# Kernel optimization log

Measured on AMD Instinct MI355X. Metric: run time of the kernel, lower is better.

The kernel has to match this reference:

```python
import jax, jax.numpy as jnp
import numpy as np

OUT = 3      # pooled output size (fmap_size//4 = 14//4 = 3)
RATIO = 2    # roi_align sampling ratio (fixed; torchvision adaptive ratio for 14/3 bins is 2)
P = 20       # num_persons


def _bilinear(fm, y, x):
    # fm: [C,H,W]; y,x broadcastable coordinate grids. torchvision aligned=False semantics.
    C, H, W = fm.shape
    y, x = jnp.broadcast_arrays(y, x)
    valid = (y > -1.0) & (y < H) & (x > -1.0) & (x < W)
    y = jnp.clip(y, 0.0, H - 1.0)
    x = jnp.clip(x, 0.0, W - 1.0)
    y0 = jnp.floor(y).astype(jnp.int32)
    x0 = jnp.floor(x).astype(jnp.int32)
    y1 = jnp.minimum(y0 + 1, H - 1)
    x1 = jnp.minimum(x0 + 1, W - 1)
    ly = y - y0
    lx = x - x0
    hy = 1.0 - ly
    hx = 1.0 - lx
    v00 = fm[:, y0, x0]
    v01 = fm[:, y0, x1]
    v10 = fm[:, y1, x0]
    v11 = fm[:, y1, x1]
    val = hy * hx * v00 + hy * lx * v01 + ly * hx * v10 + ly * lx * v11
    return jnp.where(valid, val, 0.0)  # [C, ...]


def _roi_align_one(fm, box):
    # fm: [C,H,W], box: [4] = (x1,y1,x2,y2) in feature-map coords -> [C,OUT,OUT]
    x1, y1, x2, y2 = box
    bw = (x2 - x1) / OUT
    bh = (y2 - y1) / OUT
    off = (jnp.arange(OUT * RATIO, dtype=fm.dtype) + 0.5) / RATIO  # bin-unit offsets
    xs = x1 + off * bw
    ys = y1 + off * bh
    vals = _bilinear(fm, ys[:, None], xs[None, :])  # [C, OUT*RATIO, OUT*RATIO]
    C = fm.shape[0]
    return vals.reshape(C, OUT, RATIO, OUT, RATIO).mean(axis=(2, 4))


def setup_inputs() -> dict:
    key = jax.random.key(0)
    ks = jax.random.split(key, 8)
    B, N, NB, C, FS = 128, 8, 27, 1024, 14
    fmap = jax.random.normal(ks[0], (B, C, FS, FS), jnp.float32)
    # boxes in feature-map coordinates with x1<x2, y1<y2
    lo = jax.random.uniform(ks[1], (B, N, 2), jnp.float32) * 10.0
    ext = 2.0 + jax.random.uniform(ks[2], (B, N, 2), jnp.float32) * 4.0
    hi = jnp.minimum(lo + ext, float(FS))
    boxes = jnp.concatenate([lo, hi], axis=-1)  # [B,N,4] (x1,y1,x2,y2)
    # unique person ids per frame (scatter target indices)
    pids = jax.vmap(lambda k: jax.random.permutation(k, P)[:N])(jax.random.split(ks[3], B)).astype(jnp.int32)
    w1 = jax.random.normal(ks[4], (512, C), jnp.float32) * 0.02
    w2 = jax.random.normal(ks[5], (256, 512), jnp.float32) * 0.05
    fc1_w = jax.random.normal(ks[6], (1024, 256 * OUT * OUT), jnp.float32) * 0.02
    fc1_b = jnp.zeros((1024,), jnp.float32)
    fc2_w = jax.random.normal(ks[7], (27, 1024), jnp.float32) * 0.02
    fc2_b = jnp.zeros((27,), jnp.float32)
    return {"fmap": fmap, "boxes": boxes, "pids": pids, "w1": w1, "w2": w2,
            "fc1_w": fc1_w, "fc1_b": fc1_b, "fc2_w": fc2_w, "fc2_b": fc2_b}


def _forward(fmap, boxes, pids, w1, w2, fc1_w, fc1_b, fc2_w, fc2_b):
    B, N = boxes.shape[:2]
    # per-image, per-box ROI align: [B,N,C,3,3]
    roi = jax.vmap(jax.vmap(_roi_align_one, in_axes=(None, 0)), in_axes=(0, 0))(fmap, boxes)
    # behavior_conv: two bias-free 1x1 convs (no nonlinearity between)
    h = jnp.einsum('bnchw,oc->bnohw', roi, w1)
    h = jnp.einsum('bnchw,oc->bnohw', h, w2)  # [B,N,256,3,3]
    feat = h.reshape(B, N, -1)                # [B,N,2304]
    bidx = jnp.broadcast_to(jnp.arange(B)[:, None], (B, N))
    # scatter into behavior_tensor keyed by person id (unique pids per frame -> well-defined)
    bt = jnp.zeros((B, P, feat.shape[-1]), feat.dtype).at[bidx, pids].set(feat)
    mean_b = bt.mean(axis=0)                  # [P,2304] mean over batch
    cur = bt[bidx, pids]                      # [B,N,2304]
    diff = mean_b[pids] - cur
    # behavior_fc (dropout is identity at inference)
    h1 = jax.nn.relu(jnp.einsum('bnd,hd->bnh', diff, fc1_w) + fc1_b)
    return jnp.einsum('bnh,oh->bno', h1, fc2_w) + fc2_b  # [B,N,num_behaviors]


def reference(fmap, boxes, pids, w1, w2, fc1_w, fc1_b, fc2_w, fc2_b):
    # fmap is detached and roi_align runs under no_grad in the original
    return _forward(jax.lax.stop_gradient(fmap), jax.lax.stop_gradient(boxes), pids,
                    w1, w2, fc1_w, fc1_b, fc2_w, fc2_b)
```

## Files before the change

kernel.cpp:

```cpp
#include <hip/hip_runtime.h>
#include <hip/hip_bf16.h>
#include <cstddef>
#include <cstdint>

#define B_   128
#define N_   8
#define C_   1024
#define FS_  14
#define POS_ 196
#define P_   20
#define HWC_ 9
#define CMID_ 256
#define FEATD_ 2304
#define H1_  1024
#define O_   27
#define GROWS_ (B_*POS_)

typedef __attribute__((ext_vector_type(8))) short bf16x8;
typedef __attribute__((ext_vector_type(4))) float f32x4;

__device__ __forceinline__ void gld16(const void* g, void* l) {
    __builtin_amdgcn_global_load_lds(
        (const __attribute__((address_space(1))) unsigned int*)g,
        (__attribute__((address_space(3))) unsigned int*)l, 16, 0, 0);
}

__global__ __launch_bounds__(256) void wcombine_split_kernel(
    const float* __restrict__ w1,
    const float* __restrict__ w2,
    float* __restrict__ wpart)
{
    const int tid = threadIdx.x;
    const int tx = tid & 15, ty = tid >> 4;
    const int c0 = blockIdx.x * 64;
    const int o0 = blockIdx.y * 64;
    const int kb = blockIdx.z * 64;
    __shared__ __align__(16) float As[16][68];
    __shared__ __align__(16) float Bs[16][68];
    float acc[4][4] = {};
    for (int k0 = kb; k0 < kb + 64; k0 += 16) {
        for (int i = tid; i < 64 * 16; i += 256) {
            int k = i & 15, m = i >> 4;
            As[k][m] = w2[(size_t)(o0 + m) * 512 + k0 + k];
        }
        for (int i = tid; i < 64 * 16; i += 256) {
            int n = i & 63, k = i >> 6;
            Bs[k][n] = w1[(size_t)(k0 + k) * 1024 + c0 + n];
        }
        __syncthreads();
        #pragma unroll
        for (int k = 0; k < 16; ++k) {
            float4 a = *(const float4*)&As[k][ty * 4];
            float4 b = *(const float4*)&Bs[k][tx * 4];
            float av[4] = {a.x, a.y, a.z, a.w};
            float bv[4] = {b.x, b.y, b.z, b.w};
            #pragma unroll
            for (int i = 0; i < 4; ++i)
                #pragma unroll
                for (int j = 0; j < 4; ++j)
                    acc[i][j] += av[i] * bv[j];
        }
        __syncthreads();
    }
    float* dst = wpart + (size_t)blockIdx.z * (256 * 1024);
    for (int i = 0; i < 4; ++i) {
        float4 v = make_float4(acc[i][0], acc[i][1], acc[i][2], acc[i][3]);
        *(float4*)&dst[(size_t)(o0 + ty * 4 + i) * 1024 + c0 + tx * 4] = v;
    }
}

__global__ __launch_bounds__(256) void wc_reduce_kernel(
    const float* __restrict__ wpart, __hip_bfloat16* __restrict__ Wc)
{
    int idx = blockIdx.x * 256 + threadIdx.x;
    float s = 0.f;
    #pragma unroll
    for (int z = 0; z < 8; ++z) s += wpart[(size_t)z * (256 * 1024) + idx];
    Wc[idx] = __float2bfloat16(s);
}

__global__ __launch_bounds__(256, 3) void posgemm_kernel(
    const float* __restrict__ fmap,
    const __hip_bfloat16* __restrict__ Wc,
    __hip_bfloat16* __restrict__ G)
{
    const int tid = threadIdx.x;
    const int wave = tid >> 6, lane = tid & 63;
    const int m16 = lane & 15, quad = lane >> 4;
    const int r0 = blockIdx.x * 64;

    const int r = r0 + lane;
    const int b_l = r / 196;
    const int pos_l = r - b_l * 196;
    const size_t abase = (size_t)b_l * (C_ * POS_) + pos_l;

    __shared__ __align__(16) __hip_bfloat16 As[64 * 66];
    __shared__ __align__(16) __hip_bfloat16 Bs[256 * 64];

    f32x4 acc[4][4];
    #pragma unroll
    for (int i = 0; i < 4; ++i)
        #pragma unroll
        for (int j = 0; j < 4; ++j)
            acc[i][j] = (f32x4){0.f, 0.f, 0.f, 0.f};

    for (int k0 = 0; k0 < 1024; k0 += 64) {
        #pragma unroll
        for (int jj = 0; jj < 8; ++jj) {
            int q = (wave * 8 + jj) * 64 + lane;
            int mq = q >> 3, cq = q & 7;
            int csq = cq ^ (mq & 7);
            gld16(Wc + (size_t)mq * 1024 + k0 + csq * 8,
                  (char*)Bs + (size_t)(wave * 8 + jj) * 1024);
        }
        #pragma unroll
        for (int p = 0; p < 4; ++p) {
            int cc = p * 16 + wave * 4;
            const float* fp = fmap + abase + (size_t)(k0 + cc) * POS_;
            float f0 = fp[0];
            float f1 = fp[POS_];
            float f2 = fp[2 * POS_];
            float f3 = fp[3 * POS_];
            __hip_bfloat162 q0, q1;
            q0.x = __float2bfloat16(f0); q0.y = __float2bfloat16(f1);
            q1.x = __float2bfloat16(f2); q1.y = __float2bfloat16(f3);
            *(__hip_bfloat162*)&As[lane * 66 + cc]     = q0;
            *(__hip_bfloat162*)&As[lane * 66 + cc + 2] = q1;
        }
        __syncthreads();
        #pragma unroll
        for (int ks = 0; ks < 2; ++ks) {
            bf16x8 af[4], bfv[4];
            #pragma unroll
            for (int i = 0; i < 4; ++i) {
                int m = i * 16 + m16;
                af[i] = *(const bf16x8*)&As[m * 66 + (ks * 4 + quad) * 8];
                int n = wave * 64 + i * 16 + m16;
                int cq2 = (ks * 4 + quad) ^ (n & 7);
                bfv[i] = *(const bf16x8*)&Bs[(n * 8 + cq2) * 8];
            }
            #pragma unroll
            for (int i = 0; i < 4; ++i)
                #pragma unroll
                for (int j = 0; j < 4; ++j)
                    acc[i][j] = __builtin_amdgcn_mfma_f32_16x16x32_bf16(
                        af[i], bfv[j], acc[i][j], 0, 0, 0);
        }
        __syncthreads();
    }

    #pragma unroll
    for (int i = 0; i < 4; ++i) {
        #pragma unroll
        for (int j = 0; j < 4; ++j) {
            int col = wave * 64 + j * 16 + m16;
            int rb = r0 + i * 16 + quad * 4;
            #pragma unroll
            for (int g = 0; g < 4; ++g)
                G[(size_t)(rb + g) * 256 + col] = __float2bfloat16(acc[i][j][g]);
        }
    }
}

__global__ __launch_bounds__(576) void roi2_kernel(
    const __hip_bfloat16* __restrict__ G,
    const float* __restrict__ boxes,
    float* __restrict__ feat)
{
    const int b = blockIdx.y;
    const int o0 = blockIdx.x * 64;
    const int tid = threadIdx.x;
    const int l = tid & 63;
    const int cell = tid >> 6;
    const int ch = cell / 3, cw = cell % 3;
    __shared__ __align__(16) __hip_bfloat16 Ls[POS_ * 64];

    for (int idx = tid; idx < POS_ * 8; idx += 576) {
        int p = idx >> 3, chunk = idx & 7;
        const uint4* src = (const uint4*)(G +
            ((size_t)(b * POS_ + p) * 256 + o0 + chunk * 8));
        *(uint4*)&Ls[p * 64 + chunk * 8] = *src;
    }
    __syncthreads();

    for (int n = 0; n < N_; ++n) {
        const float* bx = boxes + (size_t)(b * N_ + n) * 4;
        float x1 = bx[0], y1 = bx[1], x2 = bx[2], y2 = bx[3];
        float bw = (x2 - x1) * (1.0f / 3.0f);
        float bh = (y2 - y1) * (1.0f / 3.0f);
        float acc = 0.0f;
        #pragma unroll
        for (int si = 0; si < 2; ++si) {
            float yy = y1 + ((float)(2 * ch + si) + 0.5f) * 0.5f * bh;
            #pragma unroll
            for (int sj = 0; sj < 2; ++sj) {
                float xx = x1 + ((float)(2 * cw + sj) + 0.5f) * 0.5f * bw;
                bool valid = (yy > -1.0f) && (yy < (float)FS_) &&
                             (xx > -1.0f) && (xx < (float)FS_);
                float y = fminf(fmaxf(yy, 0.0f), (float)(FS_ - 1));
                float x = fminf(fmaxf(xx, 0.0f), (float)(FS_ - 1));
                int y0 = (int)floorf(y);
                int x0 = (int)floorf(x);
                int y1i = min(y0 + 1, FS_ - 1);
                int x1i = min(x0 + 1, FS_ - 1);
                float ly = y - (float)y0, lx = x - (float)x0;
                float hy = 1.0f - ly,     hx = 1.0f - lx;
                float v00 = __bfloat162float(Ls[(y0  * FS_ + x0 ) * 64 + l]);
                float v01 = __bfloat162float(Ls[(y0  * FS_ + x1i) * 64 + l]);
                float v10 = __bfloat162float(Ls[(y1i * FS_ + x0 ) * 64 + l]);
                float v11 = __bfloat162float(Ls[(y1i * FS_ + x1i) * 64 + l]);
                float val = hy * hx * v00 + hy * lx * v01 +
                            ly * hx * v10 + ly * lx * v11;
                acc += valid ? val : 0.0f;
            }
        }
        feat[(size_t)(b * N_ + n) * FEATD_ + cell * 256 + o0 + l] = acc * 0.25f;
    }
}

__global__ __launch_bounds__(256) void fc1_gemm_kernel(
    const __hip_bfloat16* __restrict__ A,
    const __hip_bfloat16* __restrict__ Bm,
    const float* __restrict__ bias,
    float* __restrict__ C)
{
    const int tid = threadIdx.x;
    const int wave = tid >> 6, lane = tid & 63;
    const int r0 = blockIdx.y * 64, n0 = blockIdx.x * 64;
    const int wm = (wave >> 1) * 32, wn = (wave & 1) * 32;
    const int m16 = lane & 15, quad = lane >> 4;
    const int K = FEATD_;
    __shared__ __align__(16) __hip_bfloat16 As[64 * 64];
    __shared__ __align__(16) __hip_bfloat16 Bs[64 * 64];

    f32x4 acc[2][2];
    #pragma unroll
    for (int i = 0; i < 2; ++i)
        #pragma unroll
        for (int j = 0; j < 2; ++j)
            acc[i][j] = (f32x4){0.f, 0.f, 0.f, 0.f};

    const int s0 = wave * 64 + lane;
    const int ms0 = s0 >> 3, cs0 = (s0 & 7) ^ (ms0 & 7);
    const int s1 = 256 + s0;
    const int ms1 = s1 >> 3, cs1 = (s1 & 7) ^ (ms1 & 7);
    const size_t rA0 = (size_t)(r0 + ms0) * K + cs0 * 8;
    const size_t rA1 = (size_t)(r0 + ms1) * K + cs1 * 8;
    const size_t rB0 = (size_t)(n0 + ms0) * K + cs0 * 8;
    const size_t rB1 = (size_t)(n0 + ms1) * K + cs1 * 8;

    for (int k0 = 0; k0 < K; k0 += 64) {
        gld16(A + rA0 + k0, &As[wave * 512]);
        gld16(Bm + rB0 + k0, &Bs[wave * 512]);
        gld16(A + rA1 + k0, &As[2048 + wave * 512]);
        gld16(Bm + rB1 + k0, &Bs[2048 + wave * 512]);
        __syncthreads();
        #pragma unroll
        for (int ks = 0; ks < 2; ++ks) {
            bf16x8 af[2], bfv[2];
            #pragma unroll
            for (int t = 0; t < 2; ++t) {
                int m = wm + t * 16 + m16;
                int cp = (ks * 4 + quad) ^ (m & 7);
                af[t] = *(const bf16x8*)&As[(m * 8 + cp) * 8];
                int n = wn + t * 16 + m16;
                int cq = (ks * 4 + quad) ^ (n & 7);
                bfv[t] = *(const bf16x8*)&Bs[(n * 8 + cq) * 8];
            }
            #pragma unroll
            for (int i = 0; i < 2; ++i)
                #pragma unroll
                for (int j = 0; j < 2; ++j)
                    acc[i][j] = __builtin_amdgcn_mfma_f32_16x16x32_bf16(
                        af[i], bfv[j], acc[i][j], 0, 0, 0);
        }
        __syncthreads();
    }

    #pragma unroll
    for (int i = 0; i < 2; ++i) {
        #pragma unroll
        for (int j = 0; j < 2; ++j) {
            int col = n0 + wn + j * 16 + m16;
            int rbase = r0 + wm + i * 16 + quad * 4;
            float bv = bias[col];
            #pragma unroll
            for (int g = 0; g < 4; ++g) {
                int r = rbase + g;
                float v = acc[i][j][g] + bv;
                C[(size_t)r * H1_ + col] = v > 0.f ? v : 0.f;
            }
        }
    }
}

__global__ __launch_bounds__(256) void fc1w_perm_kernel(
    const float* __restrict__ src, __hip_bfloat16* __restrict__ dst)
{
    int h = blockIdx.y;
    int d2 = blockIdx.x * 256 + threadIdx.x;
    int hw = d2 >> 8, o = d2 & 255;
    dst[(size_t)h * FEATD_ + d2] =
        __float2bfloat16(src[(size_t)h * FEATD_ + o * HWC_ + hw]);
}

__global__ __launch_bounds__(64) void invmap_kernel(
    const int* __restrict__ pids, int* __restrict__ inv)
{
    int b = blockIdx.x;
    int p = threadIdx.x;
    if (p < P_) {
        int v = -1;
        for (int n = 0; n < N_; ++n)
            if (pids[b * N_ + n] == p) v = n;
        inv[b * P_ + p] = v;
    }
}

__global__ __launch_bounds__(256) void meanb_kernel(
    const float* __restrict__ feat, const int* __restrict__ inv,
    float* __restrict__ mean_b)
{
    int p = blockIdx.x;
    int d = blockIdx.y * 256 + threadIdx.x;
    float acc = 0.0f;
    for (int b = 0; b < B_; ++b) {
        int n = inv[b * P_ + p];
        if (n >= 0) acc += feat[(size_t)(b * N_ + n) * FEATD_ + d];
    }
    mean_b[(size_t)p * FEATD_ + d] = acc * (1.0f / (float)B_);
}

__global__ __launch_bounds__(256) void diff_kernel(
    const float* __restrict__ feat, const float* __restrict__ mean_b,
    const int* __restrict__ pids, __hip_bfloat16* __restrict__ diff)
{
    int r = blockIdx.x;
    int pid = pids[r];
    const float* fr = feat + (size_t)r * FEATD_;
    const float* mr = mean_b + (size_t)pid * FEATD_;
    __hip_bfloat16* dr = diff + (size_t)r * FEATD_;
    for (int d = threadIdx.x; d < FEATD_; d += 256)
        dr[d] = __float2bfloat16(mr[d] - fr[d]);
}

__global__ __launch_bounds__(256) void fc2_kernel(
    const float* __restrict__ h1, const float* __restrict__ fc2_w,
    const float* __restrict__ fc2_b, float* __restrict__ out)
{
    int bn = blockIdx.x;
    int tid = threadIdx.x;
    __shared__ __align__(16) float row[H1_];
    __shared__ float partial[32][8];
    ((float4*)row)[tid] = ((const float4*)(h1 + (size_t)bn * H1_))[tid];
    __syncthreads();
    int o = tid >> 3, part = tid & 7;
    float acc = 0.0f;
    if (o < O_) {
        const float* wrow = fc2_w + (size_t)o * H1_ + part * 128;
        const float* hrow = row + part * 128;
        #pragma unroll 4
        for (int j = 0; j < 128; ++j) acc += hrow[j] * wrow[j];
    }
    partial[o][part] = acc;
    __syncthreads();
    if (part == 0 && o < O_) {
        float s = fc2_b[o];
        #pragma unroll
        for (int p = 0; p < 8; ++p) s += partial[o][p];
        out[(size_t)bn * O_ + o] = s;
    }
}

extern "C" void kernel_launch(void* const* d_in, const int* in_sizes, int n_in,
                              void* d_out, int out_size, void* d_ws, size_t ws_size,
                              hipStream_t stream) {
    const float* fmap  = (const float*)d_in[0];
    const float* boxes = (const float*)d_in[1];
    const int*   pids  = (const int*)  d_in[2];
    const float* w1    = (const float*)d_in[3];
    const float* w2    = (const float*)d_in[4];
    const float* fc1_w = (const float*)d_in[5];
    const float* fc1_b = (const float*)d_in[6];
    const float* fc2_w = (const float*)d_in[7];
    const float* fc2_b = (const float*)d_in[8];
    float* out = (float*)d_out;

    char* wsb = (char*)d_ws;
    __hip_bfloat16* Wc    = (__hip_bfloat16*)wsb;
    __hip_bfloat16* G     = Wc + 256 * 1024;
    __hip_bfloat16* fc1wp = G + (size_t)GROWS_ * 256;
    __hip_bfloat16* diffp = fc1wp + (size_t)H1_ * FEATD_;
    float* feat   = (float*)(diffp + (size_t)H1_ * FEATD_);
    float* mean_b = feat + (size_t)(B_ * N_) * FEATD_;
    float* h1     = mean_b + (size_t)P_ * FEATD_;
    int*   inv    = (int*)(h1 + (size_t)(B_ * N_) * H1_);
    float* wpart  = (float*)(inv + 128 * P_ + 64);

    hipLaunchKernelGGL(wcombine_split_kernel, dim3(16, 4, 8), dim3(256), 0, stream,
                       w1, w2, wpart);
    hipLaunchKernelGGL(wc_reduce_kernel, dim3(1024), dim3(256), 0, stream,
                       wpart, Wc);
    hipLaunchKernelGGL(posgemm_kernel, dim3(GROWS_ / 64), dim3(256), 0, stream,
                       fmap, Wc, G);
    hipLaunchKernelGGL(roi2_kernel, dim3(4, 128), dim3(576), 0, stream,
                       G, boxes, feat);
    hipLaunchKernelGGL(fc1w_perm_kernel, dim3(9, 1024), dim3(256), 0, stream,
                       fc1_w, fc1wp);
    hipLaunchKernelGGL(invmap_kernel, dim3(128), dim3(64), 0, stream,
                       pids, inv);
    hipLaunchKernelGGL(meanb_kernel, dim3(20, 9), dim3(256), 0, stream,
                       feat, inv, mean_b);
    hipLaunchKernelGGL(diff_kernel, dim3(1024), dim3(256), 0, stream,
                       feat, mean_b, pids, diffp);
    hipLaunchKernelGGL(fc1_gemm_kernel, dim3(16, 16), dim3(256), 0, stream,
                       diffp, fc1wp, fc1_b, h1);
    hipLaunchKernelGGL(fc2_kernel, dim3(1024), dim3(256), 0, stream,
                       h1, fc2_w, fc2_b, out);
}
```

Measured before the change: 308.3 us.

## Shrink GEMM row tiles, coalesce fc1 weight permute via LDS, unroll mean loop

```diff
diff --git a/kernel.cpp b/kernel.cpp
--- a/kernel.cpp
+++ b/kernel.cpp
@@ -79,7 +79,7 @@
     Wc[idx] = __float2bfloat16(s);
 }
 
-__global__ __launch_bounds__(256, 3) void posgemm_kernel(
+__global__ __launch_bounds__(256, 4) void posgemm_kernel(
     const float* __restrict__ fmap,
     const __hip_bfloat16* __restrict__ Wc,
     __hip_bfloat16* __restrict__ G)
@@ -87,19 +87,20 @@
     const int tid = threadIdx.x;
     const int wave = tid >> 6, lane = tid & 63;
     const int m16 = lane & 15, quad = lane >> 4;
-    const int r0 = blockIdx.x * 64;
-
-    const int r = r0 + lane;
-    const int b_l = r / 196;
-    const int pos_l = r - b_l * 196;
-    const size_t abase = (size_t)b_l * (C_ * POS_) + pos_l;
-
-    __shared__ __align__(16) __hip_bfloat16 As[64 * 66];
+    const int r0 = blockIdx.x * 32;
+
+    const int rs = r0 + (tid & 31);
+    const int b_s = rs / 196;
+    const int pos_s = rs - b_s * 196;
+    const size_t abase = (size_t)b_s * (C_ * POS_) + pos_s;
+    const int cg = (tid >> 5) * 8;
+
+    __shared__ __align__(16) __hip_bfloat16 As[32 * 66];
     __shared__ __align__(16) __hip_bfloat16 Bs[256 * 64];
 
-    f32x4 acc[4][4];
-    #pragma unroll
-    for (int i = 0; i < 4; ++i)
+    f32x4 acc[2][4];
+    #pragma unroll
+    for (int i = 0; i < 2; ++i)
         #pragma unroll
         for (int j = 0; j < 4; ++j)
             acc[i][j] = (f32x4){0.f, 0.f, 0.f, 0.f};
@@ -113,34 +114,44 @@
             gld16(Wc + (size_t)mq * 1024 + k0 + csq * 8,
                   (char*)Bs + (size_t)(wave * 8 + jj) * 1024);
         }
-        #pragma unroll
-        for (int p = 0; p < 4; ++p) {
-            int cc = p * 16 + wave * 4;
-            const float* fp = fmap + abase + (size_t)(k0 + cc) * POS_;
+        {
+            const float* fp = fmap + abase + (size_t)(k0 + cg) * POS_;
             float f0 = fp[0];
             float f1 = fp[POS_];
             float f2 = fp[2 * POS_];
             float f3 = fp[3 * POS_];
-            __hip_bfloat162 q0, q1;
-            q0.x = __float2bfloat16(f0); q0.y = __float2bfloat16(f1);
-            q1.x = __float2bfloat16(f2); q1.y = __float2bfloat16(f3);
-            *(__hip_bfloat162*)&As[lane * 66 + cc]     = q0;
-            *(__hip_bfloat162*)&As[lane * 66 + cc + 2] = q1;
+            float f4 = fp[4 * POS_];
+            float f5 = fp[5 * POS_];
+            float f6 = fp[6 * POS_];
+            float f7 = fp[7 * POS_];
+            __hip_bfloat162 p0, p1, p2, p3;
+            p0.x = __float2bfloat16(f0); p0.y = __float2bfloat16(f1);
+            p1.x = __float2bfloat16(f2); p1.y = __float2bfloat16(f3);
+            p2.x = __float2bfloat16(f4); p2.y = __float2bfloat16(f5);
+            p3.x = __float2bfloat16(f6); p3.y = __float2bfloat16(f7);
+            __hip_bfloat16* ap = &As[(tid & 31) * 66 + cg];
+            *(__hip_bfloat162*)(ap)     = p0;
+            *(__hip_bfloat162*)(ap + 2) = p1;
+            *(__hip_bfloat162*)(ap + 4) = p2;
+            *(__hip_bfloat162*)(ap + 6) = p3;
         }
         __syncthreads();
         #pragma unroll
         for (int ks = 0; ks < 2; ++ks) {
-            bf16x8 af[4], bfv[4];
-            #pragma unroll
-            for (int i = 0; i < 4; ++i) {
+            bf16x8 af[2], bfv[4];
+            #pragma unroll
+            for (int i = 0; i < 2; ++i) {
                 int m = i * 16 + m16;
                 af[i] = *(const bf16x8*)&As[m * 66 + (ks * 4 + quad) * 8];
-                int n = wave * 64 + i * 16 + m16;
+            }
+            #pragma unroll
+            for (int j = 0; j < 4; ++j) {
+                int n = wave * 64 + j * 16 + m16;
                 int cq2 = (ks * 4 + quad) ^ (n & 7);
-                bfv[i] = *(const bf16x8*)&Bs[(n * 8 + cq2) * 8];
+                bfv[j] = *(const bf16x8*)&Bs[(n * 8 + cq2) * 8];
             }
             #pragma unroll
-            for (int i = 0; i < 4; ++i)
+            for (int i = 0; i < 2; ++i)
                 #pragma unroll
                 for (int j = 0; j < 4; ++j)
                     acc[i][j] = __builtin_amdgcn_mfma_f32_16x16x32_bf16(
@@ -150,7 +161,7 @@
     }
 
     #pragma unroll
-    for (int i = 0; i < 4; ++i) {
+    for (int i = 0; i < 2; ++i) {
         #pragma unroll
         for (int j = 0; j < 4; ++j) {
             int col = wave * 64 + j * 16 + m16;
@@ -218,7 +229,7 @@
     }
 }
 
-__global__ __launch_bounds__(256) void fc1_gemm_kernel(
+__global__ __launch_bounds__(256, 4) void fc1_gemm_kernel(
     const __hip_bfloat16* __restrict__ A,
     const __hip_bfloat16* __restrict__ Bm,
     const float* __restrict__ bias,
@@ -226,70 +237,60 @@
 {
     const int tid = threadIdx.x;
     const int wave = tid >> 6, lane = tid & 63;
-    const int r0 = blockIdx.y * 64, n0 = blockIdx.x * 64;
-    const int wm = (wave >> 1) * 32, wn = (wave & 1) * 32;
+    const int r0 = blockIdx.y * 32, n0 = blockIdx.x * 64;
+    const int wm = (wave >> 1) * 16, wn = (wave & 1) * 32;
     const int m16 = lane & 15, quad = lane >> 4;
     const int K = FEATD_;
-    __shared__ __align__(16) __hip_bfloat16 As[64 * 64];
+    __shared__ __align__(16) __hip_bfloat16 As[32 * 64];
     __shared__ __align__(16) __hip_bfloat16 Bs[64 * 64];
 
-    f32x4 acc[2][2];
-    #pragma unroll
-    for (int i = 0; i < 2; ++i)
-        #pragma unroll
-        for (int j = 0; j < 2; ++j)
-            acc[i][j] = (f32x4){0.f, 0.f, 0.f, 0.f};
-
-    const int s0 = wave * 64 + lane;
-    const int ms0 = s0 >> 3, cs0 = (s0 & 7) ^ (ms0 & 7);
-    const int s1 = 256 + s0;
-    const int ms1 = s1 >> 3, cs1 = (s1 & 7) ^ (ms1 & 7);
-    const size_t rA0 = (size_t)(r0 + ms0) * K + cs0 * 8;
-    const size_t rA1 = (size_t)(r0 + ms1) * K + cs1 * 8;
-    const size_t rB0 = (size_t)(n0 + ms0) * K + cs0 * 8;
-    const size_t rB1 = (size_t)(n0 + ms1) * K + cs1 * 8;
+    f32x4 acc[2];
+    acc[0] = (f32x4){0.f, 0.f, 0.f, 0.f};
+    acc[1] = (f32x4){0.f, 0.f, 0.f, 0.f};
+
+    const int qa = wave * 64 + lane;
+    const int msA = qa >> 3, csA = (qa & 7) ^ (msA & 7);
+    const int qb1 = qa + 256;
+    const int msB1 = qb1 >> 3, csB1 = (qb1 & 7) ^ (msB1 & 7);
+    const size_t rA  = (size_t)(r0 + msA)  * K + csA  * 8;
+    const size_t rB0 = (size_t)(n0 + msA)  * K + csA  * 8;
+    const size_t rB1 = (size_t)(n0 + msB1) * K + csB1 * 8;
 
     for (int k0 = 0; k0 < K; k0 += 64) {
-        gld16(A + rA0 + k0, &As[wave * 512]);
+        gld16(A  + rA  + k0, &As[wave * 512]);
         gld16(Bm + rB0 + k0, &Bs[wave * 512]);
-        gld16(A + rA1 + k0, &As[2048 + wave * 512]);
         gld16(Bm + rB1 + k0, &Bs[2048 + wave * 512]);
         __syncthreads();
         #pragma unroll
         for (int ks = 0; ks < 2; ++ks) {
-            bf16x8 af[2], bfv[2];
+            bf16x8 af, bfv[2];
+            int m = wm + m16;
+            int cp = (ks * 4 + quad) ^ (m & 7);
+            af = *(const bf16x8*)&As[(m * 8 + cp) * 8];
             #pragma unroll
             for (int t = 0; t < 2; ++t) {
-                int m = wm + t * 16 + m16;
-                int cp = (ks * 4 + quad) ^ (m & 7);
-                af[t] = *(const bf16x8*)&As[(m * 8 + cp) * 8];
                 int n = wn + t * 16 + m16;
                 int cq = (ks * 4 + quad) ^ (n & 7);
                 bfv[t] = *(const bf16x8*)&Bs[(n * 8 + cq) * 8];
             }
             #pragma unroll
-            for (int i = 0; i < 2; ++i)
-                #pragma unroll
-                for (int j = 0; j < 2; ++j)
-                    acc[i][j] = __builtin_amdgcn_mfma_f32_16x16x32_bf16(
-                        af[i], bfv[j], acc[i][j], 0, 0, 0);
-        }
-        __syncthreads();
-    }
-
-    #pragma unroll
-    for (int i = 0; i < 2; ++i) {
-        #pragma unroll
-        for (int j = 0; j < 2; ++j) {
-            int col = n0 + wn + j * 16 + m16;
-            int rbase = r0 + wm + i * 16 + quad * 4;
-            float bv = bias[col];
-            #pragma unroll
-            for (int g = 0; g < 4; ++g) {
-                int r = rbase + g;
-                float v = acc[i][j][g] + bv;
-                C[(size_t)r * H1_ + col] = v > 0.f ? v : 0.f;
-            }
+            for (int j = 0; j < 2; ++j)
+                acc[j] = __builtin_amdgcn_mfma_f32_16x16x32_bf16(
+                    af, bfv[j], acc[j], 0, 0, 0);
+        }
+        __syncthreads();
+    }
+
+    #pragma unroll
+    for (int j = 0; j < 2; ++j) {
+        int col = n0 + wn + j * 16 + m16;
+        int rbase = r0 + wm + quad * 4;
+        float bv = bias[col];
+        #pragma unroll
+        for (int g = 0; g < 4; ++g) {
+            int r = rbase + g;
+            float v = acc[j][g] + bv;
+            C[(size_t)r * H1_ + col] = v > 0.f ? v : 0.f;
         }
     }
 }
@@ -297,11 +298,20 @@
 __global__ __launch_bounds__(256) void fc1w_perm_kernel(
     const float* __restrict__ src, __hip_bfloat16* __restrict__ dst)
 {
-    int h = blockIdx.y;
-    int d2 = blockIdx.x * 256 + threadIdx.x;
-    int hw = d2 >> 8, o = d2 & 255;
-    dst[(size_t)h * FEATD_ + d2] =
-        __float2bfloat16(src[(size_t)h * FEATD_ + o * HWC_ + hw]);
+    int h = blockIdx.x;
+    int tid = threadIdx.x;
+    __shared__ float buf[FEATD_];
+    const float* s = src + (size_t)h * FEATD_;
+    #pragma unroll
+    for (int it = 0; it < 9; ++it)
+        buf[it * 256 + tid] = s[it * 256 + tid];
+    __syncthreads();
+    __hip_bfloat16* d = dst + (size_t)h * FEATD_;
+    #pragma unroll
+    for (int it = 0; it < 9; ++it) {
+        int dd = it * 256 + tid;
+        d[dd] = __float2bfloat16(buf[tid * HWC_ + it]);
+    }
 }
 
 __global__ __launch_bounds__(64) void invmap_kernel(
@@ -324,6 +334,7 @@
     int p = blockIdx.x;
     int d = blockIdx.y * 256 + threadIdx.x;
     float acc = 0.0f;
+    #pragma unroll 4
     for (int b = 0; b < B_; ++b) {
         int n = inv[b * P_ + p];
         if (n >= 0) acc += feat[(size_t)(b * N_ + n) * FEATD_ + d];
@@ -401,11 +412,11 @@
                        w1, w2, wpart);
     hipLaunchKernelGGL(wc_reduce_kernel, dim3(1024), dim3(256), 0, stream,
                        wpart, Wc);
-    hipLaunchKernelGGL(posgemm_kernel, dim3(GROWS_ / 64), dim3(256), 0, stream,
+    hipLaunchKernelGGL(posgemm_kernel, dim3(GROWS_ / 32), dim3(256), 0, stream,
                        fmap, Wc, G);
     hipLaunchKernelGGL(roi2_kernel, dim3(4, 128), dim3(576), 0, stream,
                        G, boxes, feat);
-    hipLaunchKernelGGL(fc1w_perm_kernel, dim3(9, 1024), dim3(256), 0, stream,
+    hipLaunchKernelGGL(fc1w_perm_kernel, dim3(1024), dim3(256), 0, stream,
                        fc1_w, fc1wp);
     hipLaunchKernelGGL(invmap_kernel, dim3(128), dim3(64), 0, stream,
                        pids, inv);
@@ -413,7 +424,7 @@
                        feat, inv, mean_b);
     hipLaunchKernelGGL(diff_kernel, dim3(1024), dim3(256), 0, stream,
                        feat, mean_b, pids, diffp);
-    hipLaunchKernelGGL(fc1_gemm_kernel, dim3(16, 16), dim3(256), 0, stream,
+    hipLaunchKernelGGL(fc1_gemm_kernel, dim3(16, 32), dim3(256), 0, stream,
                        diffp, fc1wp, fc1_b, h1);
     hipLaunchKernelGGL(fc2_kernel, dim3(1024), dim3(256), 0, stream,
                        h1, fc2_w, fc2_b, out);
```

Measured after the change: 310.1 us. No clear change (+0.6%).
